# Kernel optimization log

Measured on AMD Instinct MI355X. Metric: run time of the kernel, lower is better.

Reference implementation:

```python
import jax, jax.numpy as jnp
import numpy as np

N_NODES = 50000
N_EDGES = 600000
IN_DIM = 128
HID = 128
HEADS = 2
OUT_DIM = 1
NEG_SLOPE = 0.2  # PyG GATv2Conv default leaky_relu slope


def _gatv2_layer(x, src, dst, Wl, bl, Wr, br, att, bias):
    """GATv2Conv (PyG semantics): lin_l on source, lin_r on target,
    e = att . leaky_relu(xs_j + xd_i), softmax over incoming edges of i,
    out_i = sum_j alpha_ij * xs_j, heads concatenated, plus output bias."""
    n = x.shape[0]
    xs = (x @ Wl + bl).reshape(n, HEADS, HID)   # [N,H,C] source transform
    xd = (x @ Wr + br).reshape(n, HEADS, HID)   # [N,H,C] target transform
    m = xs[src] + xd[dst]                        # [E,H,C] per-edge message
    m = jnp.where(m > 0, m, NEG_SLOPE * m)       # leaky_relu
    e = jnp.einsum('ehc,hc->eh', m, att)         # [E,H] attention logits
    emax = jax.lax.stop_gradient(
        jax.ops.segment_max(e, dst, num_segments=n))  # stable softmax shift
    a = jnp.exp(e - emax[dst])
    denom = jax.ops.segment_sum(a, dst, num_segments=n)  # [N,H]
    alpha = a / (denom[dst] + 1e-16)             # [E,H] per-dest softmax
    out = jax.ops.segment_sum(alpha[:, :, None] * xs[src], dst, num_segments=n)
    return out.reshape(n, HEADS * HID) + bias


def setup_inputs() -> dict:
    key = jax.random.key(0)
    ks = jax.random.split(key, 16)
    x = jax.random.normal(ks[0], (N_NODES, IN_DIM), dtype=jnp.float32)
    edge_index = jax.random.randint(ks[1], (2, N_EDGES), 0, N_NODES, dtype=jnp.int64)

    def lin(k, fi, fo):
        s = 1.0 / np.sqrt(fi)
        k1, k2 = jax.random.split(k)
        return (jax.random.uniform(k1, (fi, fo), jnp.float32, -s, s),
                jax.random.uniform(k2, (fo,), jnp.float32, -s, s))

    Wl1, bl1 = lin(ks[2], IN_DIM, HEADS * HID)
    Wr1, br1 = lin(ks[3], IN_DIM, HEADS * HID)
    att1 = jax.random.normal(ks[4], (HEADS, HID), jnp.float32) * (1.0 / np.sqrt(HID))
    bias1 = jnp.zeros((HEADS * HID,), jnp.float32)
    Wl2, bl2 = lin(ks[5], HEADS * HID, HEADS * HID)
    Wr2, br2 = lin(ks[6], HEADS * HID, HEADS * HID)
    att2 = jax.random.normal(ks[7], (HEADS, HID), jnp.float32) * (1.0 / np.sqrt(HID))
    bias2 = jnp.zeros((HEADS * HID,), jnp.float32)
    W3, b3 = lin(ks[8], HEADS * HID, HID)
    W4, b4 = lin(ks[9], HID, OUT_DIM)
    return {"x": x, "edge_index": edge_index,
            "Wl1": Wl1, "bl1": bl1, "Wr1": Wr1, "br1": br1, "att1": att1, "bias1": bias1,
            "Wl2": Wl2, "bl2": bl2, "Wr2": Wr2, "br2": br2, "att2": att2, "bias2": bias2,
            "W3": W3, "b3": b3, "W4": W4, "b4": b4}


def reference(x, edge_index, Wl1, bl1, Wr1, br1, att1, bias1,
              Wl2, bl2, Wr2, br2, att2, bias2, W3, b3, W4, b4):
    n = x.shape[0]
    loops = jnp.arange(n, dtype=edge_index.dtype)  # add_self_loops=True (PyG default)
    src = jnp.concatenate([edge_index[0], loops])
    dst = jnp.concatenate([edge_index[1], loops])
    h = _gatv2_layer(x, src, dst, Wl1, bl1, Wr1, br1, att1, bias1)
    h = jax.nn.relu(h)  # dropout = identity in eval mode
    h = _gatv2_layer(h, src, dst, Wl2, bl2, Wr2, br2, att2, bias2)
    h = jax.nn.relu(h)
    h = (h @ W3 + b3) @ W4 + b4  # post_mp: Linear -> Dropout(id) -> Linear
    return jax.nn.sigmoid(h)
```

## Files before the change

kernel.cpp:

```cpp
#include <hip/hip_runtime.h>
#include <hip/hip_bf16.h>
#include <hip/hip_fp16.h>
#include <math.h>


typedef short bf16x8 __attribute__((ext_vector_type(8)));
typedef float f32x4  __attribute__((ext_vector_type(4)));

#define TM 128
#define TN 128
#define GBK 64

__device__ inline void load_lds16(const void* g, void* l)
{
    __builtin_amdgcn_global_load_lds((const __attribute__((address_space(1))) void*)g,
                                     (__attribute__((address_space(3))) void*)l, 16, 0, 0);
}

__global__ __launch_bounds__(256) void gemm_mfma(
    const __hip_bfloat16* __restrict__ A, const __hip_bfloat16* __restrict__ Bt,
    const float* __restrict__ bl, const float* __restrict__ br,
    _Float16* __restrict__ xsh, float* __restrict__ xd,
    int M, int K)
{
    __shared__ char lsA[TM * GBK * 2];
    __shared__ char lsB[TN * GBK * 2];

    int t = threadIdx.x;
    int w = t >> 6, l = t & 63;
    int row0 = blockIdx.y * TM;
    int col0 = blockIdx.x * TN;

    int wrow = (w >> 1) * 64, wcol = (w & 1) * 64;
    int lr = l & 15, lh = l >> 4;

    f32x4 acc[4][4] = {};

    for (int k0 = 0; k0 < K; k0 += GBK) {
#pragma unroll
        for (int c = 0; c < 4; ++c) {
            int i = c * 256 + t;
            int r = i >> 3, p = i & 7;
            int sl = p ^ (r & 7);
            load_lds16(A  + (size_t)(row0 + r) * K + k0 + sl * 8, lsA + (c * 256 + w * 64) * 16);
            load_lds16(Bt + (size_t)(col0 + r) * K + k0 + sl * 8, lsB + (c * 256 + w * 64) * 16);
        }
        __syncthreads();
#pragma unroll
        for (int kk = 0; kk < 2; ++kk) {
            bf16x8 af[4], bg[4];
#pragma unroll
            for (int m = 0; m < 4; ++m) {
                int r = wrow + m * 16 + lr;
                int sl = (kk * 4 + lh) ^ (r & 7);
                af[m] = *(const bf16x8*)(lsA + r * 128 + sl * 16);
            }
#pragma unroll
            for (int n = 0; n < 4; ++n) {
                int r = wcol + n * 16 + lr;
                int sl = (kk * 4 + lh) ^ (r & 7);
                bg[n] = *(const bf16x8*)(lsB + r * 128 + sl * 16);
            }
#pragma unroll
            for (int m = 0; m < 4; ++m)
#pragma unroll
                for (int n = 0; n < 4; ++n)
                    acc[m][n] = __builtin_amdgcn_mfma_f32_16x16x32_bf16(af[m], bg[n], acc[m][n], 0, 0, 0);
        }
        __syncthreads();
    }

    bool is_xs = (col0 < 256);
#pragma unroll
    for (int n = 0; n < 4; ++n) {
        int col = col0 + wcol + n * 16 + lr;
        float bv = is_xs ? bl[col] : br[col - 256];
#pragma unroll
        for (int m = 0; m < 4; ++m) {
            int rbase = row0 + wrow + m * 16 + lh * 4;
#pragma unroll
            for (int j = 0; j < 4; ++j) {
                int row = rbase + j;
                if (row < M) {
                    float v = acc[m][n][j] + bv;
                    if (is_xs) xsh[(size_t)row * 256 + col] = (_Float16)v;
                    else       xd [(size_t)row * 256 + col - 256] = v;
                }
            }
        }
    }
}


__global__ void prep_wt(const float* __restrict__ Wl, const float* __restrict__ Wr,
                        __hip_bfloat16* __restrict__ Wt, int K)
{
    int idx = blockIdx.x * blockDim.x + threadIdx.x;
    if (idx >= 512 * K) return;
    int n = idx / K, k = idx - n * K;
    float v = (n < 256) ? Wl[(size_t)k * 256 + n] : Wr[(size_t)k * 256 + (n - 256)];
    Wt[idx] = __float2bfloat16(v);
}

__global__ void conv_bf16(const float* __restrict__ in, __hip_bfloat16* __restrict__ out, int n)
{
    int i = blockIdx.x * blockDim.x + threadIdx.x;
    if (i * 4 >= n) return;
    float4 v = *(const float4*)&in[i * 4];
    __hip_bfloat16 t0 = __float2bfloat16(v.x), t1 = __float2bfloat16(v.y);
    __hip_bfloat16 t2 = __float2bfloat16(v.z), t3 = __float2bfloat16(v.w);
    ushort4 pk = make_ushort4(*(unsigned short*)&t0, *(unsigned short*)&t1,
                              *(unsigned short*)&t2, *(unsigned short*)&t3);
    *(ushort4*)&out[(size_t)i * 4] = pk;
}


__global__ void count_edges(const int* __restrict__ dst, int* __restrict__ counts, int E)
{
    int i = blockIdx.x * blockDim.x + threadIdx.x;
    if (i < E) atomicAdd(&counts[dst[i]], 1);
}

__global__ __launch_bounds__(1024) void scan_kernel(
    const int* __restrict__ counts, int* __restrict__ row_ptr,
    int* __restrict__ cursor, int n)
{
    __shared__ int wsum[16];
    __shared__ int stot;
    int tid = threadIdx.x;
    int lane = tid & 63, wid = tid >> 6;
    int offset = 0;
    for (int base = 0; base < n; base += 1024) {
        int idx = base + tid;
        int v = (idx < n) ? counts[idx] : 0;
        int x = v;
#pragma unroll
        for (int off = 1; off < 64; off <<= 1) {
            int y = __shfl_up(x, off);
            if (lane >= off) x += y;
        }
        if (lane == 63) wsum[wid] = x;
        __syncthreads();
        if (tid == 0) {
            int run = 0;
#pragma unroll
            for (int i = 0; i < 16; ++i) { int tt = wsum[i]; wsum[i] = run; run += tt; }
            stot = run;
        }
        __syncthreads();
        int excl = offset + wsum[wid] + x - v;
        if (idx < n) { row_ptr[idx] = excl; cursor[idx] = excl; }
        offset += stot;
        __syncthreads();
    }
    if (tid == 0) row_ptr[n] = offset;
}

__global__ void scatter_edges(const int* __restrict__ src, const int* __restrict__ dst,
                              int* __restrict__ cursor, int* __restrict__ csr_src, int E)
{
    int i = blockIdx.x * blockDim.x + threadIdx.x;
    if (i < E) {
        int pos = atomicAdd(&cursor[dst[i]], 1);
        csr_src[pos] = src[i];
    }
}

__global__ __launch_bounds__(256) void w34_kernel(
    const float* __restrict__ W3, const float* __restrict__ b3,
    const float* __restrict__ W4, const float* __restrict__ b4,
    float* __restrict__ w34)
{
    int wid = blockIdx.x * 4 + (threadIdx.x >> 6);
    int lane = threadIdx.x & 63;
    if (wid > 256) return;
    const float* row = (wid < 256) ? &W3[(size_t)wid * 128] : b3;
    float p = row[lane] * W4[lane] + row[lane + 64] * W4[lane + 64];
#pragma unroll
    for (int off = 32; off; off >>= 1) p += __shfl_xor(p, off);
    if (lane == 0) w34[wid] = (wid < 256) ? p : (p + b4[0]);
}


template<bool FUSED>
__global__ __launch_bounds__(256) void gat_agg(
    const _Float16* __restrict__ xsh, const float* __restrict__ xd,
    const float* __restrict__ att, const float* __restrict__ bias,
    const int* __restrict__ row_ptr, const int* __restrict__ csr_src,
    __hip_bfloat16* __restrict__ outb, float* __restrict__ outf,
    const float* __restrict__ w34, int n)
{
    int node = blockIdx.x * 4 + (threadIdx.x >> 6);
    if (node >= n) return;
    int lane = threadIdx.x & 63;
    int c = lane * 4;

    float4 xdv = *(const float4*)&xd[(size_t)node * 256 + c];
    float4 atv = *(const float4*)&att[c];

    float m = -INFINITY, l = 0.f;
    float4 acc = make_float4(0.f, 0.f, 0.f, 0.f);

    int s = row_ptr[node], e = row_ptr[node + 1];
    int deg = e - s;
    int my_src = (lane < deg) ? csr_src[s + lane] : 0;

    for (int i = -1; i < deg; ++i) {
        int srcn = (i < 0) ? node : ((i < 64) ? __shfl(my_src, i) : csr_src[s + i]);
        ushort4 us = *(const ushort4*)&xsh[(size_t)srcn * 256 + c];
        float x0 = (float)(*(const _Float16*)&us.x);
        float x1 = (float)(*(const _Float16*)&us.y);
        float x2 = (float)(*(const _Float16*)&us.z);
        float x3 = (float)(*(const _Float16*)&us.w);
        float v0 = x0 + xdv.x; v0 = v0 > 0.f ? v0 : 0.2f * v0;
        float v1 = x1 + xdv.y; v1 = v1 > 0.f ? v1 : 0.2f * v1;
        float v2 = x2 + xdv.z; v2 = v2 > 0.f ? v2 : 0.2f * v2;
        float v3 = x3 + xdv.w; v3 = v3 > 0.f ? v3 : 0.2f * v3;
        float p = v0 * atv.x + v1 * atv.y + v2 * atv.z + v3 * atv.w;
#pragma unroll
        for (int off = 16; off; off >>= 1) p += __shfl_xor(p, off);

        float pm = p - m;
        if (__all(pm <= 8.f)) {
            float wgt = __expf(pm);
            l += wgt;
            acc.x += wgt * x0;
            acc.y += wgt * x1;
            acc.z += wgt * x2;
            acc.w += wgt * x3;
        } else {
            float mn = fmaxf(m, p);
            float sc = __expf(m - mn);
            float wgt = __expf(p - mn);
            l = l * sc + wgt;
            acc.x = acc.x * sc + wgt * x0;
            acc.y = acc.y * sc + wgt * x1;
            acc.z = acc.z * sc + wgt * x2;
            acc.w = acc.w * sc + wgt * x3;
            m = mn;
        }
    }
    float inv = 1.f / (l + 1e-16f);
    float4 bv = *(const float4*)&bias[c];
    float4 o;
    o.x = fmaxf(acc.x * inv + bv.x, 0.f);
    o.y = fmaxf(acc.y * inv + bv.y, 0.f);
    o.z = fmaxf(acc.z * inv + bv.z, 0.f);
    o.w = fmaxf(acc.w * inv + bv.w, 0.f);

    if (!FUSED) {
        __hip_bfloat16 t0 = __float2bfloat16(o.x), t1 = __float2bfloat16(o.y);
        __hip_bfloat16 t2 = __float2bfloat16(o.z), t3 = __float2bfloat16(o.w);
        ushort4 pk = make_ushort4(*(unsigned short*)&t0, *(unsigned short*)&t1,
                                  *(unsigned short*)&t2, *(unsigned short*)&t3);
        *(ushort4*)&outb[(size_t)node * 256 + c] = pk;
    } else {
        float4 wv = *(const float4*)&w34[c];
        float p = o.x * wv.x + o.y * wv.y + o.z * wv.z + o.w * wv.w;
#pragma unroll
        for (int off = 32; off; off >>= 1) p += __shfl_xor(p, off);
        if (lane == 0) outf[node] = 1.f / (1.f + __expf(-(p + w34[256])));
    }
}


extern "C" void kernel_launch(void* const* d_in, const int* in_sizes, int n_in,
                              void* d_out, int out_size, void* d_ws, size_t ws_size,
                              hipStream_t stream)
{
    const float* x     = (const float*)d_in[0];
    const int*   ei    = (const int*)d_in[1];
    const float* Wl1   = (const float*)d_in[2];
    const float* bl1   = (const float*)d_in[3];
    const float* Wr1   = (const float*)d_in[4];
    const float* br1   = (const float*)d_in[5];
    const float* att1  = (const float*)d_in[6];
    const float* bias1 = (const float*)d_in[7];
    const float* Wl2   = (const float*)d_in[8];
    const float* bl2   = (const float*)d_in[9];
    const float* Wr2   = (const float*)d_in[10];
    const float* br2   = (const float*)d_in[11];
    const float* att2  = (const float*)d_in[12];
    const float* bias2 = (const float*)d_in[13];
    const float* W3    = (const float*)d_in[14];
    const float* b3    = (const float*)d_in[15];
    const float* W4    = (const float*)d_in[16];
    const float* b4    = (const float*)d_in[17];

    const int N = in_sizes[0] / 128;
    const int E = in_sizes[1] / 2;
    const int Mp = ((N + TM - 1) / TM) * TM;
    const int* src = ei;
    const int* dst = ei + E;

    char* ws = (char*)d_ws;
    _Float16*       xsh     = (_Float16*)(ws + 0);
    float*          xd      = (float*)(ws + 25600000);
    __hip_bfloat16* xbf     = (__hip_bfloat16*)(ws + 76800000);
    __hip_bfloat16* hbf     = (__hip_bfloat16*)(ws + 89612288);
    __hip_bfloat16* Wt1     = (__hip_bfloat16*)(ws + 115236864);
    __hip_bfloat16* Wt2     = (__hip_bfloat16*)(ws + 115367936);
    int*            row_ptr = (int*)(ws + 115630080);
    int*            counts  = (int*)(ws + 115830144);
    int*            cursor  = (int*)(ws + 116030144);
    int*            csr_src = (int*)(ws + 116230144);
    float*          w34     = (float*)(ws + 118630144);

    hipMemsetAsync(counts, 0, N * sizeof(int), stream);
    count_edges<<<(E + 255) / 256, 256, 0, stream>>>(dst, counts, E);
    scan_kernel<<<1, 1024, 0, stream>>>(counts, row_ptr, cursor, N);
    scatter_edges<<<(E + 255) / 256, 256, 0, stream>>>(src, dst, cursor, csr_src, E);
    w34_kernel<<<65, 256, 0, stream>>>(W3, b3, W4, b4, w34);
    prep_wt<<<(512 * 128 + 255) / 256, 256, 0, stream>>>(Wl1, Wr1, Wt1, 128);
    prep_wt<<<(512 * 256 + 255) / 256, 256, 0, stream>>>(Wl2, Wr2, Wt2, 256);
    conv_bf16<<<(N * 128 / 4 + 255) / 256, 256, 0, stream>>>(x, xbf, N * 128);

    dim3 gemmGrid(512 / TN, Mp / TM);
    int aggBlocks = (N + 3) / 4;

    gemm_mfma<<<gemmGrid, 256, 0, stream>>>(xbf, Wt1, bl1, br1, xsh, xd, N, 128);
    gat_agg<false><<<aggBlocks, 256, 0, stream>>>(xsh, xd, att1, bias1, row_ptr, csr_src,
                                                  hbf, nullptr, nullptr, N);

    gemm_mfma<<<gemmGrid, 256, 0, stream>>>(hbf, Wt2, bl2, br2, xsh, xd, N, 256);
    gat_agg<true><<<aggBlocks, 256, 0, stream>>>(xsh, xd, att2, bias2, row_ptr, csr_src,
                                                 nullptr, (float*)d_out, w34, N);
}
```

Measured before the change: 476.5 us.

## Split wavefront into two edge slots in GAT aggregation and stage GEMM epilogue via LDS

The aggregation kernel now has each half-wavefront handle a different edge, with lanes loading 8 fp16 channels each. The two halves keep separate online-softmax states and merge them at the end, which halves the serial loop trip count per node. The GEMM epilogue writes the accumulators to shared memory and then issues coalesced vectorized global stores instead of scattered scalar stores. The cost is extra shuffles, a final softmax merge, and additional LDS traffic and barriers in the epilogue.

```diff
diff --git a/kernel.cpp b/kernel.cpp
--- a/kernel.cpp
+++ b/kernel.cpp
@@ -4,8 +4,10 @@
 #include <math.h>
 
 
-typedef short bf16x8 __attribute__((ext_vector_type(8)));
-typedef float f32x4  __attribute__((ext_vector_type(4)));
+typedef short    bf16x8 __attribute__((ext_vector_type(8)));
+typedef float    f32x4  __attribute__((ext_vector_type(4)));
+typedef _Float16 f16x8  __attribute__((ext_vector_type(8)));
+typedef _Float16 f16x4  __attribute__((ext_vector_type(4)));
 
 #define TM 128
 #define TN 128
@@ -23,8 +25,9 @@
     _Float16* __restrict__ xsh, float* __restrict__ xd,
     int M, int K)
 {
-    __shared__ char lsA[TM * GBK * 2];
-    __shared__ char lsB[TN * GBK * 2];
+    __shared__ char smem[32768];
+    char* lsA = smem;
+    char* lsB = smem + 16384;
 
     int t = threadIdx.x;
     int w = t >> 6, l = t & 63;
@@ -50,44 +53,65 @@
         for (int kk = 0; kk < 2; ++kk) {
             bf16x8 af[4], bg[4];
 #pragma unroll
-            for (int m = 0; m < 4; ++m) {
-                int r = wrow + m * 16 + lr;
+            for (int mm = 0; mm < 4; ++mm) {
+                int r = wrow + mm * 16 + lr;
                 int sl = (kk * 4 + lh) ^ (r & 7);
-                af[m] = *(const bf16x8*)(lsA + r * 128 + sl * 16);
+                af[mm] = *(const bf16x8*)(lsA + r * 128 + sl * 16);
             }
 #pragma unroll
-            for (int n = 0; n < 4; ++n) {
-                int r = wcol + n * 16 + lr;
+            for (int nn = 0; nn < 4; ++nn) {
+                int r = wcol + nn * 16 + lr;
                 int sl = (kk * 4 + lh) ^ (r & 7);
-                bg[n] = *(const bf16x8*)(lsB + r * 128 + sl * 16);
+                bg[nn] = *(const bf16x8*)(lsB + r * 128 + sl * 16);
             }
 #pragma unroll
-            for (int m = 0; m < 4; ++m)
-#pragma unroll
-                for (int n = 0; n < 4; ++n)
-                    acc[m][n] = __builtin_amdgcn_mfma_f32_16x16x32_bf16(af[m], bg[n], acc[m][n], 0, 0, 0);
-        }
-        __syncthreads();
-    }
-
+            for (int mm = 0; mm < 4; ++mm)
+#pragma unroll
+                for (int nn = 0; nn < 4; ++nn)
+                    acc[mm][nn] = __builtin_amdgcn_mfma_f32_16x16x32_bf16(af[mm], bg[nn], acc[mm][nn], 0, 0, 0);
+        }
+        __syncthreads();
+    }
+
+    float* stg = (float*)smem;
     bool is_xs = (col0 < 256);
-#pragma unroll
-    for (int n = 0; n < 4; ++n) {
-        int col = col0 + wcol + n * 16 + lr;
-        float bv = is_xs ? bl[col] : br[col - 256];
-#pragma unroll
-        for (int m = 0; m < 4; ++m) {
-            int rbase = row0 + wrow + m * 16 + lh * 4;
-#pragma unroll
-            for (int j = 0; j < 4; ++j) {
-                int row = rbase + j;
-                if (row < M) {
-                    float v = acc[m][n][j] + bv;
-                    if (is_xs) xsh[(size_t)row * 256 + col] = (_Float16)v;
-                    else       xd [(size_t)row * 256 + col - 256] = v;
+    int cb = (t & 31) * 4;
+    int rb = t >> 5;
+    float4 bv = is_xs ? *(const float4*)&bl[col0 + cb]
+                      : *(const float4*)&br[col0 + cb - 256];
+
+#pragma unroll
+    for (int pass = 0; pass < 2; ++pass) {
+        if ((w >> 1) == pass) {
+#pragma unroll
+            for (int mm = 0; mm < 4; ++mm)
+#pragma unroll
+                for (int nn = 0; nn < 4; ++nn)
+#pragma unroll
+                    for (int j = 0; j < 4; ++j) {
+                        int rl = mm * 16 + lh * 4 + j;
+                        int cl = wcol + nn * 16 + lr;
+                        stg[rl * 128 + cl] = acc[mm][nn][j];
+                    }
+        }
+        __syncthreads();
+#pragma unroll
+        for (int sw = 0; sw < 8; ++sw) {
+            int rl = rb + sw * 8;
+            int grow = row0 + pass * 64 + rl;
+            if (grow < M) {
+                float4 v = *(float4*)&stg[rl * 128 + cb];
+                v.x += bv.x; v.y += bv.y; v.z += bv.z; v.w += bv.w;
+                int gcol = col0 + cb;
+                if (is_xs) {
+                    f16x4 hvv = { (_Float16)v.x, (_Float16)v.y, (_Float16)v.z, (_Float16)v.w };
+                    *(f16x4*)&xsh[(size_t)grow * 256 + gcol] = hvv;
+                } else {
+                    *(float4*)&xd[(size_t)grow * 256 + gcol - 256] = v;
                 }
             }
         }
+        __syncthreads();
     }
 }
 
@@ -182,6 +206,8 @@
 }
 
 
+#define NEGBIG -1e30f
+
 template<bool FUSED>
 __global__ __launch_bounds__(256) void gat_agg(
     const _Float16* __restrict__ xsh, const float* __restrict__ xd,
@@ -193,73 +219,107 @@
     int node = blockIdx.x * 4 + (threadIdx.x >> 6);
     if (node >= n) return;
     int lane = threadIdx.x & 63;
-    int c = lane * 4;
-
-    float4 xdv = *(const float4*)&xd[(size_t)node * 256 + c];
-    float4 atv = *(const float4*)&att[c];
+    int hl = lane & 31;
+    int slot = lane >> 5;
+    int d = hl * 8;
+
+    float xdv[8], atv[8];
+    *(float4*)&xdv[0] = *(const float4*)&xd[(size_t)node * 256 + d];
+    *(float4*)&xdv[4] = *(const float4*)&xd[(size_t)node * 256 + d + 4];
+    *(float4*)&atv[0] = *(const float4*)&att[d];
+    *(float4*)&atv[4] = *(const float4*)&att[d + 4];
 
     float m = -INFINITY, l = 0.f;
-    float4 acc = make_float4(0.f, 0.f, 0.f, 0.f);
+    float acc[8] = {};
 
     int s = row_ptr[node], e = row_ptr[node + 1];
     int deg = e - s;
     int my_src = (lane < deg) ? csr_src[s + lane] : 0;
 
-    for (int i = -1; i < deg; ++i) {
-        int srcn = (i < 0) ? node : ((i < 64) ? __shfl(my_src, i) : csr_src[s + i]);
-        ushort4 us = *(const ushort4*)&xsh[(size_t)srcn * 256 + c];
-        float x0 = (float)(*(const _Float16*)&us.x);
-        float x1 = (float)(*(const _Float16*)&us.y);
-        float x2 = (float)(*(const _Float16*)&us.z);
-        float x3 = (float)(*(const _Float16*)&us.w);
-        float v0 = x0 + xdv.x; v0 = v0 > 0.f ? v0 : 0.2f * v0;
-        float v1 = x1 + xdv.y; v1 = v1 > 0.f ? v1 : 0.2f * v1;
-        float v2 = x2 + xdv.z; v2 = v2 > 0.f ? v2 : 0.2f * v2;
-        float v3 = x3 + xdv.w; v3 = v3 > 0.f ? v3 : 0.2f * v3;
-        float p = v0 * atv.x + v1 * atv.y + v2 * atv.z + v3 * atv.w;
-#pragma unroll
-        for (int off = 16; off; off >>= 1) p += __shfl_xor(p, off);
+    int iters = (deg + 2) >> 1;
+    for (int t = 0; t < iters; ++t) {
+        int item = 2 * t + slot;
+        bool act = (item <= deg);
+        int eidx = item - 1;
+        int bsrc = __shfl(my_src, eidx & 63);
+        int srcn = node;
+        if (act && item > 0)
+            srcn = (eidx < 64) ? bsrc : csr_src[s + eidx];
+
+        f16x8 hv = *(const f16x8*)&xsh[(size_t)srcn * 256 + d];
+        float xf[8];
+#pragma unroll
+        for (int j = 0; j < 8; ++j) xf[j] = (float)hv[j];
+
+        float p = 0.f;
+#pragma unroll
+        for (int j = 0; j < 8; ++j) {
+            float v = xf[j] + xdv[j];
+            v = fmaxf(v, 0.2f * v);
+            p = fmaf(v, atv[j], p);
+        }
+#pragma unroll
+        for (int off = 8; off; off >>= 1) p += __shfl_xor(p, off);
+        if (!act) p = NEGBIG;
 
         float pm = p - m;
         if (__all(pm <= 8.f)) {
             float wgt = __expf(pm);
             l += wgt;
-            acc.x += wgt * x0;
-            acc.y += wgt * x1;
-            acc.z += wgt * x2;
-            acc.w += wgt * x3;
+#pragma unroll
+            for (int j = 0; j < 8; ++j) acc[j] = fmaf(wgt, xf[j], acc[j]);
         } else {
             float mn = fmaxf(m, p);
             float sc = __expf(m - mn);
             float wgt = __expf(p - mn);
             l = l * sc + wgt;
-            acc.x = acc.x * sc + wgt * x0;
-            acc.y = acc.y * sc + wgt * x1;
-            acc.z = acc.z * sc + wgt * x2;
-            acc.w = acc.w * sc + wgt * x3;
+#pragma unroll
+            for (int j = 0; j < 8; ++j) acc[j] = fmaf(wgt, xf[j], acc[j] * sc);
             m = mn;
         }
     }
-    float inv = 1.f / (l + 1e-16f);
-    float4 bv = *(const float4*)&bias[c];
-    float4 o;
-    o.x = fmaxf(acc.x * inv + bv.x, 0.f);
-    o.y = fmaxf(acc.y * inv + bv.y, 0.f);
-    o.z = fmaxf(acc.z * inv + bv.z, 0.f);
-    o.w = fmaxf(acc.w * inv + bv.w, 0.f);
+
+    float mo = __shfl_xor(m, 32);
+    float lo = __shfl_xor(l, 32);
+    float mt = fmaxf(m, mo);
+    float sa = __expf(m - mt);
+    float sb = __expf(mo - mt);
+    float lt = l * sa + lo * sb;
+    float om[8];
+#pragma unroll
+    for (int j = 0; j < 8; ++j)
+        om[j] = acc[j] * sa + __shfl_xor(acc[j], 32) * sb;
+
+    float inv = 1.f / (lt + 1e-16f);
+    float bvv[8];
+    *(float4*)&bvv[0] = *(const float4*)&bias[d];
+    *(float4*)&bvv[4] = *(const float4*)&bias[d + 4];
+    float o[8];
+#pragma unroll
+    for (int j = 0; j < 8; ++j)
+        o[j] = fmaxf(fmaf(om[j], inv, bvv[j]), 0.f);
 
     if (!FUSED) {
-        __hip_bfloat16 t0 = __float2bfloat16(o.x), t1 = __float2bfloat16(o.y);
-        __hip_bfloat16 t2 = __float2bfloat16(o.z), t3 = __float2bfloat16(o.w);
-        ushort4 pk = make_ushort4(*(unsigned short*)&t0, *(unsigned short*)&t1,
-                                  *(unsigned short*)&t2, *(unsigned short*)&t3);
-        *(ushort4*)&outb[(size_t)node * 256 + c] = pk;
+        if (lane < 32) {
+            uint u[4];
+#pragma unroll
+            for (int j = 0; j < 4; ++j) {
+                __hip_bfloat16 a = __float2bfloat16(o[2 * j]);
+                __hip_bfloat16 b = __float2bfloat16(o[2 * j + 1]);
+                u[j] = (uint)(*(unsigned short*)&a) | ((uint)(*(unsigned short*)&b) << 16);
+            }
+            *(uint4*)&outb[(size_t)node * 256 + d] = make_uint4(u[0], u[1], u[2], u[3]);
+        }
     } else {
-        float4 wv = *(const float4*)&w34[c];
-        float p = o.x * wv.x + o.y * wv.y + o.z * wv.z + o.w * wv.w;
-#pragma unroll
-        for (int off = 32; off; off >>= 1) p += __shfl_xor(p, off);
-        if (lane == 0) outf[node] = 1.f / (1.f + __expf(-(p + w34[256])));
+        float wv[8];
+        *(float4*)&wv[0] = *(const float4*)&w34[d];
+        *(float4*)&wv[4] = *(const float4*)&w34[d + 4];
+        float pp = 0.f;
+#pragma unroll
+        for (int j = 0; j < 8; ++j) pp = fmaf(o[j], wv[j], pp);
+#pragma unroll
+        for (int off = 16; off; off >>= 1) pp += __shfl_xor(pp, off);
+        if (lane == 0) outf[node] = 1.f / (1.f + __expf(-(pp + w34[256])));
     }
 }
 
```

Result: faster. 416.8 us (-12.5%).
